# Kernel optimization log

Measured on AMD Instinct MI355X. Metric: run time of the kernel, lower is better.

The kernel has to match this reference:

```python
import jax, jax.numpy as jnp
import numpy as np

SAMPLES = 8    # batch of sets
N = 1024       # set size == rows of the permutation-closed index matrix
K = 16         # number of distinct weight-sharing groups
M = N // K     # columns per group per row (rectangular splits)
CI = 128       # channels_in
CO = 256       # channels_out


def setup_inputs() -> dict:
    key = jax.random.key(0)
    kx, kw = jax.random.split(key)
    x = jax.random.normal(kx, (SAMPLES, N, CI), dtype=jnp.float32)
    # weightParameter: [k, channels_out, channels_in]
    W = jax.random.normal(kw, (K, CO, CI), dtype=jnp.float32)
    # Rebuild the circulant group structure that __init__ derives from
    # running_weight_matrix: row j of `indices` is roll(base, j), so the
    # columns of group g in row j are (pos_g + j) mod N.
    base = np.repeat(np.arange(K), M)                      # indices row 0, [N]
    pos = np.stack([np.where(base == g)[0] for g in range(K)])  # [K, M]
    splits = (pos[:, None, :] + np.arange(N)[None, :, None]) % N  # [K, N, M]
    return {"x": x, "W": W, "splits": jnp.asarray(splits, jnp.int32)}


def reference(x, W, splits):
    # sum-pool branch: result = sum_g ( sum_m x[:, splits[g]] ) @ W[g].T
    def body(acc, group):
        w, sp = group                      # w: [CO, CI], sp: [N, M]
        pooled = x[:, sp].sum(axis=2)      # gather [S, N, M, CI] -> [S, N, CI]
        return acc + jnp.einsum('snc,oc->sno', pooled, w), None

    init = jnp.zeros((x.shape[0], splits.shape[1], W.shape[1]), dtype=x.dtype)
    out, _ = jax.lax.scan(body, init, (W, splits))
    return out                             # [S, N, CO]
```

## Files before the change

kernel.cpp:

```cpp
#include <hip/hip_runtime.h>
#include <hip/hip_bf16.h>

#define S_   8
#define N_   1024
#define KG_  16
#define MW_  64
#define CI_  128
#define CO_  256

typedef __attribute__((ext_vector_type(8))) short bf16x8;
typedef __attribute__((ext_vector_type(4))) float f32x4;

__global__ __launch_bounds__(256) void win_kernel(const float* __restrict__ x,
                                                  const float* __restrict__ W,
                                                  __hip_bfloat16* __restrict__ win,
                                                  __hip_bfloat16* __restrict__ Wb) {
    __shared__ float lds[96][CI_];
    const int b   = blockIdx.x;
    const int tid = threadIdx.x;

    {
        const int wi = (b * 256 + tid) * 8;
        const float4 v0 = *(const float4*)&W[wi];
        const float4 v1 = *(const float4*)&W[wi + 4];
        union { unsigned short u[8]; uint4 v; } o;
        __hip_bfloat16 h;
        h = __float2bfloat16(v0.x); o.u[0] = *(unsigned short*)&h;
        h = __float2bfloat16(v0.y); o.u[1] = *(unsigned short*)&h;
        h = __float2bfloat16(v0.z); o.u[2] = *(unsigned short*)&h;
        h = __float2bfloat16(v0.w); o.u[3] = *(unsigned short*)&h;
        h = __float2bfloat16(v1.x); o.u[4] = *(unsigned short*)&h;
        h = __float2bfloat16(v1.y); o.u[5] = *(unsigned short*)&h;
        h = __float2bfloat16(v1.z); o.u[6] = *(unsigned short*)&h;
        h = __float2bfloat16(v1.w); o.u[7] = *(unsigned short*)&h;
        *(uint4*)&Wb[wi] = o.v;
    }

    const int s   = b >> 5;
    const int t0  = (b & 31) << 5;
    const float* xs = x + (size_t)s * N_ * CI_;

    for (int e = tid * 4; e < 96 * CI_; e += 256 * 4) {
        const int r = e >> 7;
        const int c = e & (CI_ - 1);
        *(float4*)&lds[r][c] = *(const float4*)&xs[((t0 + r) & (N_ - 1)) * CI_ + c];
    }
    __syncthreads();

    const int c  = tid & (CI_ - 1);
    const int tb = (tid >> 7) << 4;
    float s0 = 0.f, s1 = 0.f, s2 = 0.f, s3 = 0.f;
    #pragma unroll
    for (int m = 0; m < MW_; m += 4) {
        s0 += lds[tb + m + 0][c];
        s1 += lds[tb + m + 1][c];
        s2 += lds[tb + m + 2][c];
        s3 += lds[tb + m + 3][c];
    }
    float w = (s0 + s1) + (s2 + s3);
    __hip_bfloat16* wo = win + (size_t)s * (2 * N_) * CI_;
    {
        const int row = t0 + tb;
        const __hip_bfloat16 hv = __float2bfloat16(w);
        wo[row * CI_ + c] = hv;
        wo[(row + N_) * CI_ + c] = hv;
    }
    #pragma unroll
    for (int t = 1; t < 16; ++t) {
        w += lds[tb + t - 1 + MW_][c] - lds[tb + t - 1][c];
        const int row = t0 + tb + t;
        const __hip_bfloat16 hv = __float2bfloat16(w);
        wo[row * CI_ + c] = hv;
        wo[(row + N_) * CI_ + c] = hv;
    }
}

#define KSTEPS 16

__global__ __launch_bounds__(256, 2) void gemm_kernel(const __hip_bfloat16* __restrict__ winb,
                                                      const __hip_bfloat16* __restrict__ Wb,
                                                      float* __restrict__ out) {
    __shared__ __align__(16) unsigned short smem[32768];

    const int tid  = threadIdx.x;
    const int l    = tid & 63;
    const int wv   = tid >> 6;
    const int pw   = wv & 1;
    const int pipe = wv >> 1;
    const int s    = blockIdx.x & 7;
    const int rem  = blockIdx.x >> 3;
    const int n0   = (rem & 15) << 6;
    const int o0   = (rem >> 4) << 6;

    const int fr = l & 15;
    const int kq = l >> 4;
    const int rl = l >> 3;
    const int ps = l & 7;

    const unsigned short* winp = (const unsigned short*)winb
                               + ((size_t)s * 2 * N_ + n0) * CI_;
    const unsigned short* Wp   = (const unsigned short*)Wb;

#define AELEM(P, B) (smem + ((P) * 2 + (B)) * 4096)
#define BELEM(P, B) (smem + 16384 + ((P) * 2 + (B)) * 4096)

    f32x4 acc[4][2];
    #pragma unroll
    for (int i = 0; i < 4; ++i)
        #pragma unroll
        for (int j = 0; j < 2; ++j)
            acc[i][j] = f32x4{0.f, 0.f, 0.f, 0.f};

    auto stage = [&](int t, int buf) {
        const int g  = pipe * 8 + (t >> 1);
        const int ch = (t & 1) << 6;
        unsigned short* Ab = AELEM(pipe, buf);
        unsigned short* Bb = BELEM(pipe, buf);
        #pragma unroll
        for (int q = 0; q < 4; ++q) {
            const int row = (pw * 4 + q) * 8 + rl;
            const int ss  = ps ^ (row & 7);
            const unsigned short* src = winp + (g * MW_ + row) * CI_ + ch + ss * 8;
            __builtin_amdgcn_global_load_lds((const __attribute__((address_space(1))) void*)src,
                                             (__attribute__((address_space(3))) void*)(Ab + ((pw * 4 + q) * 8) * 64),
                                             16, 0, 0);
        }
        #pragma unroll
        for (int q = 0; q < 4; ++q) {
            const int row = (pw * 4 + q) * 8 + rl;
            const int ss  = ps ^ (row & 7);
            const unsigned short* src = Wp + ((g * CO_ + o0 + row) * CI_) + ch + ss * 8;
            __builtin_amdgcn_global_load_lds((const __attribute__((address_space(1))) void*)src,
                                             (__attribute__((address_space(3))) void*)(Bb + ((pw * 4 + q) * 8) * 64),
                                             16, 0, 0);
        }
    };

    stage(0, 0);

    for (int t = 0; t < KSTEPS; ++t) {
        const int cur = t & 1;
        if (t < KSTEPS - 1) {
            stage(t + 1, cur ^ 1);
            asm volatile("s_waitcnt vmcnt(8)" ::: "memory");
        } else {
            asm volatile("s_waitcnt vmcnt(0)" ::: "memory");
        }
        __builtin_amdgcn_sched_barrier(0);
        __builtin_amdgcn_s_barrier();

        const unsigned short* Ab = AELEM(pipe, cur);
        const unsigned short* Bb = BELEM(pipe, cur);
        #pragma unroll
        for (int ks = 0; ks < 2; ++ks) {
            const int sl = ks * 4 + kq;
            bf16x8 af[4], bfg[2];
            #pragma unroll
            for (int i = 0; i < 4; ++i) {
                const int ar = i * 16 + fr;
                af[i] = *(const bf16x8*)&Ab[ar * 64 + ((sl ^ (ar & 7)) * 8)];
            }
            #pragma unroll
            for (int j = 0; j < 2; ++j) {
                const int br = pw * 32 + j * 16 + fr;
                bfg[j] = *(const bf16x8*)&Bb[br * 64 + ((sl ^ (br & 7)) * 8)];
            }
            #pragma unroll
            for (int i = 0; i < 4; ++i)
                #pragma unroll
                for (int j = 0; j < 2; ++j)
                    acc[i][j] = __builtin_amdgcn_mfma_f32_16x16x32_bf16(af[i], bfg[j], acc[i][j], 0, 0, 0);
        }
        __builtin_amdgcn_sched_barrier(0);
        __builtin_amdgcn_s_barrier();
    }

    float* red = (float*)smem;
    #pragma unroll
    for (int i = 0; i < 4; ++i)
        #pragma unroll
        for (int j = 0; j < 2; ++j)
            #pragma unroll
            for (int r = 0; r < 4; ++r)
                red[((pipe * 64) + (i * 16 + kq * 4 + r)) * 68 + pw * 32 + j * 16 + fr]
                    = acc[i][j][r];

    __syncthreads();

    const int row = tid >> 2;
    const int cb  = (tid & 3) << 4;
    float* op = out + ((size_t)(s * N_ + n0 + row) * CO_) + o0 + cb;
    #pragma unroll
    for (int q = 0; q < 4; ++q) {
        const f32x4 v0 = *(const f32x4*)&red[(row) * 68 + cb + q * 4];
        const f32x4 v1 = *(const f32x4*)&red[(64 + row) * 68 + cb + q * 4];
        *(f32x4*)&op[q * 4] = v0 + v1;
    }
}

extern "C" void kernel_launch(void* const* d_in, const int* in_sizes, int n_in,
                              void* d_out, int out_size, void* d_ws, size_t ws_size,
                              hipStream_t stream) {
    const float* x = (const float*)d_in[0];
    const float* W = (const float*)d_in[1];

    __hip_bfloat16* winb = (__hip_bfloat16*)d_ws;
    __hip_bfloat16* Wbb  = (__hip_bfloat16*)((char*)d_ws +
                              (size_t)S_ * 2 * N_ * CI_ * sizeof(__hip_bfloat16));
    float* out = (float*)d_out;

    win_kernel<<<256, 256, 0, stream>>>(x, W, winb, Wbb);
    gemm_kernel<<<512, 256, 0, stream>>>(winb, Wbb, out);
}
```

Baseline: 82.06 us.

## Switch GEMM to single-wave 32x32 tiles without split-K reduction

New measurement: 87.29 us. +6.4%, slower.

```diff
diff --git a/kernel.cpp b/kernel.cpp
--- a/kernel.cpp
+++ b/kernel.cpp
@@ -75,22 +75,21 @@
     }
 }
 
-#define KSTEPS 16
+#define KSTEPS 32
+#define ATILE 2048
+#define BTILE 2048
 
-__global__ __launch_bounds__(256, 2) void gemm_kernel(const __hip_bfloat16* __restrict__ winb,
-                                                      const __hip_bfloat16* __restrict__ Wb,
-                                                      float* __restrict__ out) {
-    __shared__ __align__(16) unsigned short smem[32768];
+__global__ __launch_bounds__(64, 2) void gemm_kernel(const __hip_bfloat16* __restrict__ winb,
+                                                     const __hip_bfloat16* __restrict__ Wb,
+                                                     float* __restrict__ out) {
+    __shared__ __align__(16) unsigned short Alds[2 * ATILE];
+    __shared__ __align__(16) unsigned short Blds[2 * BTILE];
 
-    const int tid  = threadIdx.x;
-    const int l    = tid & 63;
-    const int wv   = tid >> 6;
-    const int pw   = wv & 1;
-    const int pipe = wv >> 1;
-    const int s    = blockIdx.x & 7;
-    const int rem  = blockIdx.x >> 3;
-    const int n0   = (rem & 15) << 6;
-    const int o0   = (rem >> 4) << 6;
+    const int l   = threadIdx.x;
+    const int s   = blockIdx.x & 7;
+    const int rem = blockIdx.x >> 3;
+    const int n0  = (rem & 31) << 5;
+    const int o0  = (rem >> 5) << 5;
 
     const int fr = l & 15;
     const int kq = l >> 4;
@@ -101,37 +100,34 @@
                                + ((size_t)s * 2 * N_ + n0) * CI_;
     const unsigned short* Wp   = (const unsigned short*)Wb;
 
-#define AELEM(P, B) (smem + ((P) * 2 + (B)) * 4096)
-#define BELEM(P, B) (smem + 16384 + ((P) * 2 + (B)) * 4096)
-
-    f32x4 acc[4][2];
+    f32x4 acc[2][2];
     #pragma unroll
-    for (int i = 0; i < 4; ++i)
+    for (int i = 0; i < 2; ++i)
         #pragma unroll
         for (int j = 0; j < 2; ++j)
             acc[i][j] = f32x4{0.f, 0.f, 0.f, 0.f};
 
     auto stage = [&](int t, int buf) {
-        const int g  = pipe * 8 + (t >> 1);
+        const int g  = t >> 1;
         const int ch = (t & 1) << 6;
-        unsigned short* Ab = AELEM(pipe, buf);
-        unsigned short* Bb = BELEM(pipe, buf);
+        unsigned short* Ab = Alds + buf * ATILE;
+        unsigned short* Bb = Blds + buf * BTILE;
         #pragma unroll
         for (int q = 0; q < 4; ++q) {
-            const int row = (pw * 4 + q) * 8 + rl;
+            const int row = q * 8 + rl;
             const int ss  = ps ^ (row & 7);
             const unsigned short* src = winp + (g * MW_ + row) * CI_ + ch + ss * 8;
             __builtin_amdgcn_global_load_lds((const __attribute__((address_space(1))) void*)src,
-                                             (__attribute__((address_space(3))) void*)(Ab + ((pw * 4 + q) * 8) * 64),
+                                             (__attribute__((address_space(3))) void*)(Ab + (q * 8) * 64),
                                              16, 0, 0);
         }
         #pragma unroll
         for (int q = 0; q < 4; ++q) {
-            const int row = (pw * 4 + q) * 8 + rl;
+            const int row = q * 8 + rl;
             const int ss  = ps ^ (row & 7);
             const unsigned short* src = Wp + ((g * CO_ + o0 + row) * CI_) + ch + ss * 8;
             __builtin_amdgcn_global_load_lds((const __attribute__((address_space(1))) void*)src,
-                                             (__attribute__((address_space(3))) void*)(Bb + ((pw * 4 + q) * 8) * 64),
+                                             (__attribute__((address_space(3))) void*)(Bb + (q * 8) * 64),
                                              16, 0, 0);
         }
     };
@@ -147,55 +143,40 @@
             asm volatile("s_waitcnt vmcnt(0)" ::: "memory");
         }
         __builtin_amdgcn_sched_barrier(0);
-        __builtin_amdgcn_s_barrier();
 
-        const unsigned short* Ab = AELEM(pipe, cur);
-        const unsigned short* Bb = BELEM(pipe, cur);
+        const unsigned short* Ab = Alds + cur * ATILE;
+        const unsigned short* Bb = Blds + cur * BTILE;
         #pragma unroll
         for (int ks = 0; ks < 2; ++ks) {
             const int sl = ks * 4 + kq;
-            bf16x8 af[4], bfg[2];
+            bf16x8 af[2], bfg[2];
             #pragma unroll
-            for (int i = 0; i < 4; ++i) {
+            for (int i = 0; i < 2; ++i) {
                 const int ar = i * 16 + fr;
                 af[i] = *(const bf16x8*)&Ab[ar * 64 + ((sl ^ (ar & 7)) * 8)];
             }
             #pragma unroll
             for (int j = 0; j < 2; ++j) {
-                const int br = pw * 32 + j * 16 + fr;
+                const int br = j * 16 + fr;
                 bfg[j] = *(const bf16x8*)&Bb[br * 64 + ((sl ^ (br & 7)) * 8)];
             }
             #pragma unroll
-            for (int i = 0; i < 4; ++i)
+            for (int i = 0; i < 2; ++i)
                 #pragma unroll
                 for (int j = 0; j < 2; ++j)
                     acc[i][j] = __builtin_amdgcn_mfma_f32_16x16x32_bf16(af[i], bfg[j], acc[i][j], 0, 0, 0);
         }
         __builtin_amdgcn_sched_barrier(0);
-        __builtin_amdgcn_s_barrier();
     }
 
-    float* red = (float*)smem;
+    float* op = out + ((size_t)(s * N_ + n0) * CO_) + o0;
     #pragma unroll
-    for (int i = 0; i < 4; ++i)
+    for (int i = 0; i < 2; ++i)
         #pragma unroll
         for (int j = 0; j < 2; ++j)
             #pragma unroll
             for (int r = 0; r < 4; ++r)
-                red[((pipe * 64) + (i * 16 + kq * 4 + r)) * 68 + pw * 32 + j * 16 + fr]
-                    = acc[i][j][r];
-
-    __syncthreads();
-
-    const int row = tid >> 2;
-    const int cb  = (tid & 3) << 4;
-    float* op = out + ((size_t)(s * N_ + n0 + row) * CO_) + o0 + cb;
-    #pragma unroll
-    for (int q = 0; q < 4; ++q) {
-        const f32x4 v0 = *(const f32x4*)&red[(row) * 68 + cb + q * 4];
-        const f32x4 v1 = *(const f32x4*)&red[(64 + row) * 68 + cb + q * 4];
-        *(f32x4*)&op[q * 4] = v0 + v1;
-    }
+                op[(i * 16 + kq * 4 + r) * CO_ + j * 16 + fr] = acc[i][j][r];
 }
 
 extern "C" void kernel_launch(void* const* d_in, const int* in_sizes, int n_in,
@@ -210,5 +191,5 @@
     float* out = (float*)d_out;
 
     win_kernel<<<256, 256, 0, stream>>>(x, W, winb, Wbb);
-    gemm_kernel<<<512, 256, 0, stream>>>(winb, Wbb, out);
+    gemm_kernel<<<2048, 64, 0, stream>>>(winb, Wbb, out);
 }
```
